# Kernel optimization log

Measured on AMD Instinct MI355X. Metric: run time of the kernel, lower is better.

## Reference

```python
import jax, jax.numpy as jnp
import numpy as np

E, T, K, H, I = 16, 512, 8, 2048, 1024  # experts, tokens, top-k, hidden, ffn half-width


def setup_inputs() -> dict:
    key = jax.random.key(0)
    ks = jax.random.split(key, 8)
    x = jax.random.normal(ks[0], (T, H), dtype=jnp.float32)
    expert_ids = jax.random.randint(ks[1], (T, K), 0, E, dtype=jnp.int32)
    # int8-valued weights stored as int32 (exactly representable)
    gmm1_weight = jax.random.randint(ks[2], (E, H, 2 * I), -127, 128, dtype=jnp.int32)
    gmm2_weight = jax.random.randint(ks[3], (E, I, H), -127, 128, dtype=jnp.int32)
    gmm1_weight_scale = jax.random.uniform(ks[4], (E, 2 * I), dtype=jnp.float32) * 1e-3
    gmm2_weight_scale = jax.random.uniform(ks[5], (E, H), dtype=jnp.float32) * 1e-3
    smooth_scales = jax.random.uniform(ks[6], (E, H), dtype=jnp.float32)
    expert_scales = jax.random.uniform(ks[7], (T, K), dtype=jnp.float32)
    return {"x": x, "expert_ids": expert_ids, "gmm1_weight": gmm1_weight,
            "gmm1_weight_scale": gmm1_weight_scale, "gmm2_weight": gmm2_weight,
            "gmm2_weight_scale": gmm2_weight_scale, "smooth_scales": smooth_scales,
            "expert_scales": expert_scales}


def _dynamic_quant(v):
    # per-token symmetric dynamic quant to int8 range (quant_mode=2 / quant_mode=1)
    s = jnp.max(jnp.abs(v), axis=-1, keepdims=True) / 127.0
    q = jnp.clip(jnp.round(v / s), -128.0, 127.0)  # kept in f32; values are exact small ints
    return q, s


def _grouped_mm(a, w, e_flat):
    # grouped GEMM: out[i] = a[i] @ w[e_flat[i]]. Disjoint expert masks -> masked full GEMMs summed.
    out = jnp.zeros((a.shape[0], w.shape[-1]), dtype=a.dtype)
    for e in range(w.shape[0]):
        mask = (e_flat == e)[:, None]
        out = out + jnp.where(mask, a, 0.0) @ w[e]
    return out


def reference(x, expert_ids, gmm1_weight, gmm1_weight_scale, gmm2_weight,
              gmm2_weight_scale, smooth_scales, expert_scales):
    # --- dispatch: per-token dynamic int8 quant + replicate each token K times ---
    xq, s0 = _dynamic_quant(x)                 # [T,H], [T,1]
    e_flat = expert_ids.reshape(-1)            # [T*K]
    xq_e = jnp.repeat(xq, K, axis=0)           # [T*K,H]
    s0_e = jnp.repeat(s0, K, axis=0)           # [T*K,1] == dynamic_scales / activation_scale
    w1 = gmm1_weight.astype(jnp.float32)       # int8 GEMM emulated exactly in f32
    w2 = gmm2_weight.astype(jnp.float32)
    # --- grouped GEMM 1 -> int32 accumulator values ---
    y1_i32 = _grouped_mm(xq_e, w1, e_flat)     # [T*K,2I]
    # --- fused dequant + SwiGLU (activate_left) + per-token dynamic requant ---
    y1f = y1_i32 * gmm1_weight_scale[e_flat] * s0_e
    act = jax.nn.silu(y1f[:, :I]) * y1f[:, I:]
    aq, s1 = _dynamic_quant(act)               # [T*K,I], [T*K,1]
    # --- grouped GEMM 2 + dequant (per-channel weight scale * per-token scale) ---
    y2_i32 = _grouped_mm(aq, w2, e_flat)       # [T*K,H]
    y2 = y2_i32 * gmm2_weight_scale[e_flat] * s1
    # --- combine: weighted sum over the K expert copies of each token ---
    out = jnp.einsum('tkh,tk->th', y2.reshape(T, K, H), expert_scales)
    return out
```

## Files before the change

kernel.cpp:

```cpp
#include <hip/hip_runtime.h>
#include <hip/hip_bf16.h>
#include <stdint.h>

#define E_   16
#define T_   512
#define KTOP 8
#define H_   2048
#define I_   1024
#define TK_  4096

typedef __attribute__((ext_vector_type(4))) int i32x4;

#define OFF_CNT     0
#define OFF_ROWMAX  4096
#define OFF_XQ      32768
#define OFF_S0      (OFF_XQ + T_*H_)
#define OFF_S1      (OFF_S0 + 4096)
#define OFF_LIST    (OFF_S1 + TK_*4)
#define OFF_ACT     (OFF_LIST + E_*TK_*4)
#define OFF_AQ      (OFF_ACT + (size_t)TK_*I_*4)
#define OFF_Y2      (OFF_AQ + (size_t)TK_*I_)

#define SCHEDB() __builtin_amdgcn_sched_barrier(0)
#define VMCNT26() asm volatile("s_waitcnt vmcnt(26)" ::: "memory")
#define LGKM0()   asm volatile("s_waitcnt lgkmcnt(0)" ::: "memory")
#define BAR()     __builtin_amdgcn_s_barrier()

__global__ void k_zero(unsigned int* __restrict__ p) {
  int i = blockIdx.x * 256 + threadIdx.x;
  if (i < 5120) p[i] = 0;
}

__global__ void k_quant(const float* __restrict__ x, signed char* __restrict__ xq,
                        float* __restrict__ s0, const int* __restrict__ eids,
                        unsigned int* __restrict__ counts, int* __restrict__ row_list) {
  int t = blockIdx.x, tid = threadIdx.x;
  if (tid < KTOP) {
    int e = eids[t * KTOP + tid];
    int pos = (int)atomicAdd(&counts[e], 1u);
    row_list[e * TK_ + pos] = t * KTOP + tid;
  }
  const float4* xr = (const float4*)(x + (size_t)t * H_);
  float4 a = xr[tid * 2 + 0], b = xr[tid * 2 + 1];
  float m = fmaxf(
      fmaxf(fmaxf(fabsf(a.x), fabsf(a.y)), fmaxf(fabsf(a.z), fabsf(a.w))),
      fmaxf(fmaxf(fabsf(b.x), fabsf(b.y)), fmaxf(fabsf(b.z), fabsf(b.w))));
  for (int o = 32; o > 0; o >>= 1) m = fmaxf(m, __shfl_xor(m, o));
  __shared__ float wm[4];
  if ((tid & 63) == 0) wm[tid >> 6] = m;
  __syncthreads();
  m = fmaxf(fmaxf(wm[0], wm[1]), fmaxf(wm[2], wm[3]));
  float s = m / 127.0f;
  if (!(s > 0.f)) s = 1.0f;
  if (tid == 0) s0[t] = s;
  float v[8] = {a.x, a.y, a.z, a.w, b.x, b.y, b.z, b.w};
  unsigned int lo = 0, hi = 0;
#pragma unroll
  for (int j = 0; j < 4; ++j) {
    float qf = fminf(fmaxf(rintf(v[j] / s), -128.f), 127.f);
    lo |= ((unsigned)((int)qf & 0xFF)) << (8 * j);
  }
#pragma unroll
  for (int j = 0; j < 4; ++j) {
    float qf = fminf(fmaxf(rintf(v[4 + j] / s), -128.f), 127.f);
    hi |= ((unsigned)((int)qf & 0xFF)) << (8 * j);
  }
  ((uint2*)(xq + (size_t)t * H_))[tid] = make_uint2(lo, hi);
}

#define BM_   320
#define WSTR  2048

#define PACKW(SRC, DST) do {                                              \
    i32x4 pk_;                                                            \
    _Pragma("unroll")                                                     \
    for (int d_ = 0; d_ < 4; ++d_)                                        \
      pk_[d_] = ((SRC)[4*d_] & 0xFF) | (((SRC)[4*d_+1] & 0xFF) << 8) |    \
                (((SRC)[4*d_+2] & 0xFF) << 16) | ((SRC)[4*d_+3] << 24);   \
    *(i32x4*)(DST) = pk_;                                                 \
  } while (0)

#define LOADB(BANK, TT)                                                   \
    _Pragma("unroll")                                                     \
    for (int j_ = 0; j_ < 16; ++j_)                                       \
      BANK[j_] = bsrc[(size_t)((TT) * 64 + j_) * WSTR];

#define LOADAR(BANK, TT)                                                  \
    _Pragma("unroll")                                                     \
    for (int i_ = 0; i_ < 5; ++i_)                                        \
      BANK[i_] = *(const i32x4*)(gA[i_] + (TT) * 64);

#define MFMAS(ABANK, P)                                                   \
    _Pragma("unroll")                                                     \
    for (int n_ = 0; n_ < 4; ++n_) {                                      \
      i32x4 bf_ = *(const i32x4*)(bsm + (P) * 4096 + l4 * 1024 +          \
                                  (n_ * 16 + l15) * 16);                  \
      _Pragma("unroll")                                                   \
      for (int i_ = 0; i_ < 5; ++i_)                                      \
        acc[i_][n_] = __builtin_amdgcn_mfma_i32_16x16x64_i8(              \
            ABANK[i_], bf_, acc[i_][n_], 0, 0, 0);                        \
    }

#define TILE(TT, P, ABANK, BBANK, PKBANK, NT, LAST) do {                  \
    int tn_ = (TT) + 2; if (tn_ > (NT) - 1) tn_ = (NT) - 1;               \
    SCHEDB();                                                             \
    LOADB(BBANK, tn_);                                                    \
    SCHEDB();                                                             \
    MFMAS(ABANK, P);                                                      \
    SCHEDB();                                                             \
    LOADAR(ABANK, tn_);                                                   \
    SCHEDB();                                                             \
    if (!(LAST)) {                                                        \
      VMCNT26(); SCHEDB();                                                \
      PACKW(PKBANK, bsm + ((P) ^ 1) * 4096 + bkg * 1024 + bc * 16);       \
      LGKM0(); BAR(); SCHEDB();                                           \
    }                                                                     \
  } while (0)

__launch_bounds__(256, 2)
__global__ void k_gemm1(const signed char* __restrict__ xq, const int* __restrict__ w1,
                        const float* __restrict__ ws1, const float* __restrict__ s0,
                        const unsigned int* __restrict__ counts,
                        const int* __restrict__ row_list,
                        float* __restrict__ act, unsigned int* __restrict__ rowmax) {
  __shared__ alignas(16) char bsm[2 * 4096];
  int e = blockIdx.y;
  int cnt = (int)counts[e];
  if (cnt == 0) return;
  int p0 = blockIdx.x * 32;
  const int* rl = row_list + e * TK_;
  const int* we = w1 + (size_t)e * H_ * (2 * I_);
  const float* wsc = ws1 + (size_t)e * (2 * I_);

  int tid = threadIdx.x, w = tid >> 6, lane = tid & 63;
  int l15 = lane & 15, l4 = lane >> 4;
  int bc = tid & 63, bkg = tid >> 6;
  int bgcol = (bc < 32) ? (p0 + bc) : (I_ + p0 + (bc - 32));
  const int* bsrc = we + (size_t)(bkg * 16) * WSTR + bgcol;

  const int NT = H_ / 64;
  int nch = (cnt + BM_ - 1) / BM_;
  for (int ch = 0; ch < nch; ++ch) {
    if (ch) { BAR(); }
    int rbase = ch * BM_;
    const signed char* gA[5];
#pragma unroll
    for (int i = 0; i < 5; ++i) {
      int gr = rbase + w * 80 + i * 16 + l15;
      int tok = rl[gr < cnt ? gr : 0] >> 3;
      gA[i] = xq + (size_t)tok * H_ + l4 * 16;
    }
    i32x4 acc[5][4];
#pragma unroll
    for (int i = 0; i < 5; ++i)
#pragma unroll
      for (int n = 0; n < 4; ++n) acc[i][n] = (i32x4)(0);

    i32x4 aR0[5], aR1[5];
    int bR0[16], bR1[16];
    SCHEDB();
    LOADB(bR0, 0);
    SCHEDB();
    LOADAR(aR0, 0);
    LOADAR(aR1, 1);
    SCHEDB();
    LOADB(bR1, 1);
    SCHEDB();
    VMCNT26(); SCHEDB();
    PACKW(bR0, bsm + bkg * 1024 + bc * 16);
    LGKM0(); BAR(); SCHEDB();

    for (int t = 0; t < NT; t += 2) {
      TILE(t,     0, aR0, bR0, bR1, NT, false);
      TILE(t + 1, 1, aR1, bR1, bR0, NT, (t + 2 >= NT));
    }

#pragma unroll
    for (int mi = 0; mi < 5; ++mi) {
#pragma unroll
      for (int r = 0; r < 4; ++r) {
        int gr = rbase + w * 80 + mi * 16 + l4 * 4 + r;
        bool valid = gr < cnt;
        int irow = rl[valid ? gr : 0];
        float s0v = s0[irow >> 3];
        float rowm = 0.f, av0 = 0.f, av1 = 0.f;
#pragma unroll
        for (int n = 0; n < 2; ++n) {
          int colL = p0 + n * 16 + l15;
          float yl = (float)acc[mi][n][r] * wsc[colL] * s0v;
          float yr = (float)acc[mi][n + 2][r] * wsc[I_ + colL] * s0v;
          float actv = (yl / (1.f + expf(-yl))) * yr;
          if (n == 0) av0 = actv; else av1 = actv;
          rowm = fmaxf(rowm, fabsf(actv));
        }
        rowm = fmaxf(rowm, __shfl_xor(rowm, 1));
        rowm = fmaxf(rowm, __shfl_xor(rowm, 2));
        rowm = fmaxf(rowm, __shfl_xor(rowm, 4));
        rowm = fmaxf(rowm, __shfl_xor(rowm, 8));
        if (valid) {
          act[(size_t)irow * I_ + p0 + l15] = av0;
          act[(size_t)irow * I_ + p0 + 16 + l15] = av1;
          if (l15 == 0) atomicMax(rowmax + irow, __float_as_uint(rowm));
        }
      }
    }
  }
}

__global__ void k_requant(const float* __restrict__ act, const unsigned int* __restrict__ rowmax,
                          signed char* __restrict__ aq, float* __restrict__ s1) {
  int i = blockIdx.x, tid = threadIdx.x;
  float m = __uint_as_float(rowmax[i]);
  float s = (m > 0.f) ? (m / 127.0f) : 1.0f;
  if (tid == 0) s1[i] = s;
  float4 v = ((const float4*)(act + (size_t)i * I_))[tid];
  float vv[4] = {v.x, v.y, v.z, v.w};
  unsigned int pk = 0;
#pragma unroll
  for (int j = 0; j < 4; ++j) {
    float qf = fminf(fmaxf(rintf(vv[j] / s), -128.f), 127.f);
    pk |= ((unsigned)((int)qf & 0xFF)) << (8 * j);
  }
  ((unsigned int*)(aq + (size_t)i * I_))[tid] = pk;
}

__launch_bounds__(256, 2)
__global__ void k_gemm2(const signed char* __restrict__ aq, const int* __restrict__ w2,
                        const float* __restrict__ ws2, const float* __restrict__ s1,
                        const float* __restrict__ es,
                        const unsigned int* __restrict__ counts,
                        const int* __restrict__ row_list,
                        __hip_bfloat16* __restrict__ y2h) {
  __shared__ alignas(16) char bsm[2 * 4096];
  int e = blockIdx.y;
  int cnt = (int)counts[e];
  if (cnt == 0) return;
  int n0 = blockIdx.x * 64;
  const int* rl = row_list + e * TK_;
  const int* we = w2 + (size_t)e * I_ * H_;
  const float* wsc = ws2 + (size_t)e * H_;

  int tid = threadIdx.x, w = tid >> 6, lane = tid & 63;
  int l15 = lane & 15, l4 = lane >> 4;
  int bc = tid & 63, bkg = tid >> 6;
  const int* bsrc = we + (size_t)(bkg * 16) * WSTR + n0 + bc;

  const int NT = I_ / 64;
  int nch = (cnt + BM_ - 1) / BM_;
  for (int ch = 0; ch < nch; ++ch) {
    if (ch) { BAR(); }
    int rbase = ch * BM_;
    const signed char* gA[5];
#pragma unroll
    for (int i = 0; i < 5; ++i) {
      int gr = rbase + w * 80 + i * 16 + l15;
      gA[i] = aq + (size_t)rl[gr < cnt ? gr : 0] * I_ + l4 * 16;
    }
    i32x4 acc[5][4];
#pragma unroll
    for (int i = 0; i < 5; ++i)
#pragma unroll
      for (int n = 0; n < 4; ++n) acc[i][n] = (i32x4)(0);

    i32x4 aR0[5], aR1[5];
    int bR0[16], bR1[16];
    SCHEDB();
    LOADB(bR0, 0);
    SCHEDB();
    LOADAR(aR0, 0);
    LOADAR(aR1, 1);
    SCHEDB();
    LOADB(bR1, 1);
    SCHEDB();
    VMCNT26(); SCHEDB();
    PACKW(bR0, bsm + bkg * 1024 + bc * 16);
    LGKM0(); BAR(); SCHEDB();

    for (int t = 0; t < NT; t += 2) {
      TILE(t,     0, aR0, bR0, bR1, NT, false);
      TILE(t + 1, 1, aR1, bR1, bR0, NT, (t + 2 >= NT));
    }

#pragma unroll
    for (int mi = 0; mi < 5; ++mi) {
#pragma unroll
      for (int r = 0; r < 4; ++r) {
        int gr = rbase + w * 80 + mi * 16 + l4 * 4 + r;
        if (gr < cnt) {
          int irow = rl[gr];
          float sc = s1[irow] * es[irow];
#pragma unroll
          for (int n = 0; n < 4; ++n) {
            int c = n0 + n * 16 + l15;
            float v = (float)acc[mi][n][r] * wsc[c] * sc;
            y2h[(size_t)irow * H_ + c] = __float2bfloat16(v);
          }
        }
      }
    }
  }
}

__global__ void k_combine(const __hip_bfloat16* __restrict__ y2h, float* __restrict__ out) {
  int idx = blockIdx.x * 256 + threadIdx.x;
  int t = idx >> 8;
  int h0 = (idx & 255) * 8;
  float s[8];
#pragma unroll
  for (int j = 0; j < 8; ++j) s[j] = 0.f;
#pragma unroll
  for (int k = 0; k < KTOP; ++k) {
    const __hip_bfloat16* p = y2h + ((size_t)(t * KTOP + k) * H_ + h0);
    uint4 u = *(const uint4*)p;
    const __hip_bfloat16* b = (const __hip_bfloat16*)&u;
#pragma unroll
    for (int j = 0; j < 8; ++j) s[j] += __bfloat162float(b[j]);
  }
  float4 o0 = make_float4(s[0], s[1], s[2], s[3]);
  float4 o1 = make_float4(s[4], s[5], s[6], s[7]);
  float4* dst = (float4*)(out + (size_t)t * H_ + h0);
  dst[0] = o0; dst[1] = o1;
}

extern "C" void kernel_launch(void* const* d_in, const int* in_sizes, int n_in,
                              void* d_out, int out_size, void* d_ws, size_t ws_size,
                              hipStream_t stream) {
  const float* x   = (const float*)d_in[0];
  const int*   eid = (const int*)d_in[1];
  const int*   w1  = (const int*)d_in[2];
  const float* ws1 = (const float*)d_in[3];
  const int*   w2  = (const int*)d_in[4];
  const float* ws2 = (const float*)d_in[5];
  const float* es  = (const float*)d_in[7];
  float* out = (float*)d_out;
  char* ws = (char*)d_ws;

  unsigned int*  counts   = (unsigned int*)(ws + OFF_CNT);
  unsigned int*  rowmax   = (unsigned int*)(ws + OFF_ROWMAX);
  signed char*   xq       = (signed char*)(ws + OFF_XQ);
  float*         s0       = (float*)(ws + OFF_S0);
  float*         s1       = (float*)(ws + OFF_S1);
  int*           row_list = (int*)(ws + OFF_LIST);
  float*         act      = (float*)(ws + OFF_ACT);
  signed char*   aq       = (signed char*)(ws + OFF_AQ);
  __hip_bfloat16* y2h     = (__hip_bfloat16*)(ws + OFF_Y2);

  k_zero<<<20, 256, 0, stream>>>((unsigned int*)ws);
  k_quant<<<T_, 256, 0, stream>>>(x, xq, s0, eid, counts, row_list);
  k_gemm1<<<dim3(32, E_), 256, 0, stream>>>(xq, w1, ws1, s0, counts, row_list, act, rowmax);
  k_requant<<<TK_, 256, 0, stream>>>(act, rowmax, aq, s1);
  k_gemm2<<<dim3(32, E_), 256, 0, stream>>>(aq, w2, ws2, s1, es, counts, row_list, y2h);
  k_combine<<<(T_ * H_ / 8) / 256, 256, 0, stream>>>(y2h, out);
}
```

Baseline: 183.4 us.

## Stage gathered A rows into LDS via direct global-to-LDS loads with 512-thread blocks

Both grouped GEMMs now use 512-thread blocks (8 waves, BM 384, 48 rows per wave). The gathered activation rows are copied straight into a double-buffered, XOR-swizzled LDS tile with global_load_lds, where previously each wave held them in registers. The B-weight load is split so each wave loads 8 rows and packs 8 bytes. The aim is lower register pressure, higher occupancy and more latency hiding for the A gather, at the cost of more LDS (56KB per block) and a more complex swizzle and wait scheme that could break correctness or limit residency. The chunk-start barrier was removed, which risks a race between chunks.

After: 290.5 us. 58.4% more time.

```diff
diff --git a/kernel.cpp b/kernel.cpp
--- a/kernel.cpp
+++ b/kernel.cpp
@@ -22,9 +22,15 @@
 #define OFF_Y2      (OFF_AQ + (size_t)TK_*I_)
 
 #define SCHEDB() __builtin_amdgcn_sched_barrier(0)
-#define VMCNT26() asm volatile("s_waitcnt vmcnt(26)" ::: "memory")
-#define LGKM0()   asm volatile("s_waitcnt lgkmcnt(0)" ::: "memory")
-#define BAR()     __builtin_amdgcn_s_barrier()
+#define VMCNT8() asm volatile("s_waitcnt vmcnt(8)" ::: "memory")
+#define LGKM0()  asm volatile("s_waitcnt lgkmcnt(0)" ::: "memory")
+#define BAR()    __builtin_amdgcn_s_barrier()
+
+__device__ __forceinline__ void g2l16(const void* g, void* l) {
+  __builtin_amdgcn_global_load_lds(
+      (const __attribute__((address_space(1))) void*)g,
+      (__attribute__((address_space(3))) void*)l, 16, 0, 0);
+}
 
 __global__ void k_zero(unsigned int* __restrict__ p) {
   int i = blockIdx.x * 256 + threadIdx.x;
@@ -68,62 +74,84 @@
   ((uint2*)(xq + (size_t)t * H_))[tid] = make_uint2(lo, hi);
 }
 
-#define BM_   320
-#define WSTR  2048
-
-#define PACKW(SRC, DST) do {                                              \
-    i32x4 pk_;                                                            \
+#define BM_    384
+#define WSTR   2048
+#define ABUFB  24576
+#define BBASE  49152
+#define LDSSZ  57344
+
+#define PACK8(SRC, DSTPTR) do {                                           \
+    uint2 u_;                                                             \
+    u_.x = ((SRC)[0] & 0xFF) | (((SRC)[1] & 0xFF) << 8) |                 \
+           (((SRC)[2] & 0xFF) << 16) | ((SRC)[3] << 24);                  \
+    u_.y = ((SRC)[4] & 0xFF) | (((SRC)[5] & 0xFF) << 8) |                 \
+           (((SRC)[6] & 0xFF) << 16) | ((SRC)[7] << 24);                  \
+    *(uint2*)(DSTPTR) = u_;                                               \
+  } while (0)
+
+#define LOADB8(BANK, TT)                                                  \
     _Pragma("unroll")                                                     \
-    for (int d_ = 0; d_ < 4; ++d_)                                        \
-      pk_[d_] = ((SRC)[4*d_] & 0xFF) | (((SRC)[4*d_+1] & 0xFF) << 8) |    \
-                (((SRC)[4*d_+2] & 0xFF) << 16) | ((SRC)[4*d_+3] << 24);   \
-    *(i32x4*)(DST) = pk_;                                                 \
-  } while (0)
-
-#define LOADB(BANK, TT)                                                   \
+    for (int j_ = 0; j_ < 8; ++j_)                                        \
+      BANK[j_] = bsrc[(size_t)((TT) * 64 + j_) * WSTR];
+
+#define STAGEA(TT, BUF)                                                   \
     _Pragma("unroll")                                                     \
-    for (int j_ = 0; j_ < 16; ++j_)                                       \
-      BANK[j_] = bsrc[(size_t)((TT) * 64 + j_) * WSTR];
-
-#define LOADAR(BANK, TT)                                                  \
-    _Pragma("unroll")                                                     \
-    for (int i_ = 0; i_ < 5; ++i_)                                        \
-      BANK[i_] = *(const i32x4*)(gA[i_] + (TT) * 64);
-
-#define MFMAS(ABANK, P)                                                   \
-    _Pragma("unroll")                                                     \
-    for (int n_ = 0; n_ < 4; ++n_) {                                      \
-      i32x4 bf_ = *(const i32x4*)(bsm + (P) * 4096 + l4 * 1024 +          \
-                                  (n_ * 16 + l15) * 16);                  \
+    for (int s_ = 0; s_ < 3; ++s_)                                        \
+      g2l16(gAr[s_] + (TT) * 64, smem + (BUF) * ABUFB + s_ * 8192 + w * 1024);
+
+#define MFMAS(P)                                                          \
+    do {                                                                  \
+      i32x4 af_[3];                                                       \
       _Pragma("unroll")                                                   \
-      for (int i_ = 0; i_ < 5; ++i_)                                      \
-        acc[i_][n_] = __builtin_amdgcn_mfma_i32_16x16x64_i8(              \
-            ABANK[i_], bf_, acc[i_][n_], 0, 0, 0);                        \
-    }
-
-#define TILE(TT, P, ABANK, BBANK, PKBANK, NT, LAST) do {                  \
-    int tn_ = (TT) + 2; if (tn_ > (NT) - 1) tn_ = (NT) - 1;               \
-    SCHEDB();                                                             \
-    LOADB(BBANK, tn_);                                                    \
-    SCHEDB();                                                             \
-    MFMAS(ABANK, P);                                                      \
-    SCHEDB();                                                             \
-    LOADAR(ABANK, tn_);                                                   \
+      for (int mi_ = 0; mi_ < 3; ++mi_)                                   \
+        af_[mi_] = *(const i32x4*)(smem + (P) * ABUFB + aoff[mi_]);       \
+      _Pragma("unroll")                                                   \
+      for (int n_ = 0; n_ < 4; ++n_) {                                    \
+        i32x4 bf_ = *(const i32x4*)(smem + BBASE + (P) * 4096 +           \
+                                    l4 * 1024 + (n_ * 16 + l15) * 16);    \
+        _Pragma("unroll")                                                 \
+        for (int mi_ = 0; mi_ < 3; ++mi_)                                 \
+          acc[mi_][n_] = __builtin_amdgcn_mfma_i32_16x16x64_i8(           \
+              af_[mi_], bf_, acc[mi_][n_], 0, 0, 0);                      \
+      }                                                                   \
+    } while (0)
+
+#define TILE(TT, P, BBANK, PKBANK, NT, LAST) do {                         \
+    if (!(LAST)) { STAGEA((TT) + 1, (P) ^ 1); }                           \
     SCHEDB();                                                             \
     if (!(LAST)) {                                                        \
-      VMCNT26(); SCHEDB();                                                \
-      PACKW(PKBANK, bsm + ((P) ^ 1) * 4096 + bkg * 1024 + bc * 16);       \
+      int tn_ = (TT) + 2; if (tn_ > (NT) - 1) tn_ = (NT) - 1;             \
+      LOADB8(BBANK, tn_);                                                 \
+    }                                                                     \
+    SCHEDB();                                                             \
+    MFMAS(P);                                                             \
+    SCHEDB();                                                             \
+    if (!(LAST)) {                                                        \
+      VMCNT8(); SCHEDB();                                                 \
+      PACK8(PKBANK, smem + BBASE + ((P) ^ 1) * 4096 + pdst);              \
       LGKM0(); BAR(); SCHEDB();                                           \
     }                                                                     \
   } while (0)
 
-__launch_bounds__(256, 2)
+#define GEMM_PRO()                                                        \
+    SCHEDB();                                                             \
+    STAGEA(0, 0);                                                         \
+    SCHEDB();                                                             \
+    LOADB8(bRA, 0);                                                       \
+    SCHEDB();                                                             \
+    LOADB8(bRB, 1);                                                       \
+    SCHEDB();                                                             \
+    VMCNT8(); SCHEDB();                                                   \
+    PACK8(bRA, smem + BBASE + pdst);                                      \
+    LGKM0(); BAR(); SCHEDB();
+
+__launch_bounds__(512, 4)
 __global__ void k_gemm1(const signed char* __restrict__ xq, const int* __restrict__ w1,
                         const float* __restrict__ ws1, const float* __restrict__ s0,
                         const unsigned int* __restrict__ counts,
                         const int* __restrict__ row_list,
                         float* __restrict__ act, unsigned int* __restrict__ rowmax) {
-  __shared__ alignas(16) char bsm[2 * 4096];
+  __shared__ alignas(16) char smem[LDSSZ];
   int e = blockIdx.y;
   int cnt = (int)counts[e];
   if (cnt == 0) return;
@@ -134,52 +162,52 @@
 
   int tid = threadIdx.x, w = tid >> 6, lane = tid & 63;
   int l15 = lane & 15, l4 = lane >> 4;
-  int bc = tid & 63, bkg = tid >> 6;
-  int bgcol = (bc < 32) ? (p0 + bc) : (I_ + p0 + (bc - 32));
-  const int* bsrc = we + (size_t)(bkg * 16) * WSTR + bgcol;
+
+  int bgcol = (lane < 32) ? (p0 + lane) : (I_ + p0 + (lane - 32));
+  const int* bsrc = we + (size_t)(w * 8) * WSTR + bgcol;
+  const int pdst = (w >> 1) * 1024 + lane * 16 + (w & 1) * 8;
+
+  int aR[3], akc;
+  akc = ((tid >> 2) & 3) ^ ((tid >> 4) & 3);
+#pragma unroll
+  for (int s = 0; s < 3; ++s) aR[s] = s * 128 + ((tid >> 4) << 2) + (tid & 3);
+
+  int aoff[3];
+#pragma unroll
+  for (int mi = 0; mi < 3; ++mi) {
+    int R = w * 48 + mi * 16 + l15;
+    aoff[mi] = ((R >> 2) << 8) + ((l4 ^ ((R >> 2) & 3)) << 6) + ((R & 3) << 4);
+  }
 
   const int NT = H_ / 64;
   int nch = (cnt + BM_ - 1) / BM_;
   for (int ch = 0; ch < nch; ++ch) {
-    if (ch) { BAR(); }
     int rbase = ch * BM_;
-    const signed char* gA[5];
-#pragma unroll
-    for (int i = 0; i < 5; ++i) {
-      int gr = rbase + w * 80 + i * 16 + l15;
+    const signed char* gAr[3];
+#pragma unroll
+    for (int s = 0; s < 3; ++s) {
+      int gr = rbase + aR[s];
       int tok = rl[gr < cnt ? gr : 0] >> 3;
-      gA[i] = xq + (size_t)tok * H_ + l4 * 16;
-    }
-    i32x4 acc[5][4];
-#pragma unroll
-    for (int i = 0; i < 5; ++i)
+      gAr[s] = xq + (size_t)tok * H_ + akc * 16;
+    }
+    i32x4 acc[3][4];
+#pragma unroll
+    for (int i = 0; i < 3; ++i)
 #pragma unroll
       for (int n = 0; n < 4; ++n) acc[i][n] = (i32x4)(0);
 
-    i32x4 aR0[5], aR1[5];
-    int bR0[16], bR1[16];
-    SCHEDB();
-    LOADB(bR0, 0);
-    SCHEDB();
-    LOADAR(aR0, 0);
-    LOADAR(aR1, 1);
-    SCHEDB();
-    LOADB(bR1, 1);
-    SCHEDB();
-    VMCNT26(); SCHEDB();
-    PACKW(bR0, bsm + bkg * 1024 + bc * 16);
-    LGKM0(); BAR(); SCHEDB();
-
+    int bRA[8], bRB[8];
+    GEMM_PRO();
     for (int t = 0; t < NT; t += 2) {
-      TILE(t,     0, aR0, bR0, bR1, NT, false);
-      TILE(t + 1, 1, aR1, bR1, bR0, NT, (t + 2 >= NT));
-    }
-
-#pragma unroll
-    for (int mi = 0; mi < 5; ++mi) {
+      TILE(t,     0, bRA, bRB, NT, false);
+      TILE(t + 1, 1, bRB, bRA, NT, (t + 2 >= NT));
+    }
+
+#pragma unroll
+    for (int mi = 0; mi < 3; ++mi) {
 #pragma unroll
       for (int r = 0; r < 4; ++r) {
-        int gr = rbase + w * 80 + mi * 16 + l4 * 4 + r;
+        int gr = rbase + w * 48 + mi * 16 + l4 * 4 + r;
         bool valid = gr < cnt;
         int irow = rl[valid ? gr : 0];
         float s0v = s0[irow >> 3];
@@ -224,14 +252,14 @@
   ((unsigned int*)(aq + (size_t)i * I_))[tid] = pk;
 }
 
-__launch_bounds__(256, 2)
+__launch_bounds__(512, 4)
 __global__ void k_gemm2(const signed char* __restrict__ aq, const int* __restrict__ w2,
                         const float* __restrict__ ws2, const float* __restrict__ s1,
                         const float* __restrict__ es,
                         const unsigned int* __restrict__ counts,
                         const int* __restrict__ row_list,
                         __hip_bfloat16* __restrict__ y2h) {
-  __shared__ alignas(16) char bsm[2 * 4096];
+  __shared__ alignas(16) char smem[LDSSZ];
   int e = blockIdx.y;
   int cnt = (int)counts[e];
   if (cnt == 0) return;
@@ -242,50 +270,50 @@
 
   int tid = threadIdx.x, w = tid >> 6, lane = tid & 63;
   int l15 = lane & 15, l4 = lane >> 4;
-  int bc = tid & 63, bkg = tid >> 6;
-  const int* bsrc = we + (size_t)(bkg * 16) * WSTR + n0 + bc;
+
+  const int* bsrc = we + (size_t)(w * 8) * WSTR + n0 + lane;
+  const int pdst = (w >> 1) * 1024 + lane * 16 + (w & 1) * 8;
+
+  int aR[3], akc;
+  akc = ((tid >> 2) & 3) ^ ((tid >> 4) & 3);
+#pragma unroll
+  for (int s = 0; s < 3; ++s) aR[s] = s * 128 + ((tid >> 4) << 2) + (tid & 3);
+
+  int aoff[3];
+#pragma unroll
+  for (int mi = 0; mi < 3; ++mi) {
+    int R = w * 48 + mi * 16 + l15;
+    aoff[mi] = ((R >> 2) << 8) + ((l4 ^ ((R >> 2) & 3)) << 6) + ((R & 3) << 4);
+  }
 
   const int NT = I_ / 64;
   int nch = (cnt + BM_ - 1) / BM_;
   for (int ch = 0; ch < nch; ++ch) {
-    if (ch) { BAR(); }
     int rbase = ch * BM_;
-    const signed char* gA[5];
-#pragma unroll
-    for (int i = 0; i < 5; ++i) {
-      int gr = rbase + w * 80 + i * 16 + l15;
-      gA[i] = aq + (size_t)rl[gr < cnt ? gr : 0] * I_ + l4 * 16;
-    }
-    i32x4 acc[5][4];
-#pragma unroll
-    for (int i = 0; i < 5; ++i)
+    const signed char* gAr[3];
+#pragma unroll
+    for (int s = 0; s < 3; ++s) {
+      int gr = rbase + aR[s];
+      gAr[s] = aq + (size_t)rl[gr < cnt ? gr : 0] * I_ + akc * 16;
+    }
+    i32x4 acc[3][4];
+#pragma unroll
+    for (int i = 0; i < 3; ++i)
 #pragma unroll
       for (int n = 0; n < 4; ++n) acc[i][n] = (i32x4)(0);
 
-    i32x4 aR0[5], aR1[5];
-    int bR0[16], bR1[16];
-    SCHEDB();
-    LOADB(bR0, 0);
-    SCHEDB();
-    LOADAR(aR0, 0);
-    LOADAR(aR1, 1);
-    SCHEDB();
-    LOADB(bR1, 1);
-    SCHEDB();
-    VMCNT26(); SCHEDB();
-    PACKW(bR0, bsm + bkg * 1024 + bc * 16);
-    LGKM0(); BAR(); SCHEDB();
-
+    int bRA[8], bRB[8];
+    GEMM_PRO();
     for (int t = 0; t < NT; t += 2) {
-      TILE(t,     0, aR0, bR0, bR1, NT, false);
-      TILE(t + 1, 1, aR1, bR1, bR0, NT, (t + 2 >= NT));
-    }
-
-#pragma unroll
-    for (int mi = 0; mi < 5; ++mi) {
+      TILE(t,     0, bRA, bRB, NT, false);
+      TILE(t + 1, 1, bRB, bRA, NT, (t + 2 >= NT));
+    }
+
+#pragma unroll
+    for (int mi = 0; mi < 3; ++mi) {
 #pragma unroll
       for (int r = 0; r < 4; ++r) {
-        int gr = rbase + w * 80 + mi * 16 + l4 * 4 + r;
+        int gr = rbase + w * 48 + mi * 16 + l4 * 4 + r;
         if (gr < cnt) {
           int irow = rl[gr];
           float sc = s1[irow] * es[irow];
@@ -347,8 +375,8 @@
 
   k_zero<<<20, 256, 0, stream>>>((unsigned int*)ws);
   k_quant<<<T_, 256, 0, stream>>>(x, xq, s0, eid, counts, row_list);
-  k_gemm1<<<dim3(32, E_), 256, 0, stream>>>(xq, w1, ws1, s0, counts, row_list, act, rowmax);
+  k_gemm1<<<dim3(32, E_), 512, 0, stream>>>(xq, w1, ws1, s0, counts, row_list, act, rowmax);
   k_requant<<<TK_, 256, 0, stream>>>(act, rowmax, aq, s1);
-  k_gemm2<<<dim3(32, E_), 256, 0, stream>>>(aq, w2, ws2, s1, es, counts, row_list, y2h);
+  k_gemm2<<<dim3(32, E_), 512, 0, stream>>>(aq, w2, ws2, s1, es, counts, row_list, y2h);
   k_combine<<<(T_ * H_ / 8) / 256, 256, 0, stream>>>(y2h, out);
 }
```

## Halve GEMM N-tile width to double grid and raise occupancy

Applied to the files above, without the earlier changes.

Both grouped GEMM kernels now compute 32-wide (gemm1: 16 left + 16 right columns) output tiles instead of 64, doubling the grid to 64x16 blocks and raising launch bounds to 4 waves per SIMD. Each thread loads 8 weight rows instead of 16, with a new LDS packing layout and a matching vmcnt wait. The final tile also skips its redundant prefetch loads. The aim is to fill more CUs and hide memory latency, at the cost of reloading the A (activation) rows twice as often per expert.

Result: slower. 361.9 us (+97.3%).

```diff
diff --git a/kernel.cpp b/kernel.cpp
--- a/kernel.cpp
+++ b/kernel.cpp
@@ -21,8 +21,8 @@
 #define OFF_AQ      (OFF_ACT + (size_t)TK_*I_*4)
 #define OFF_Y2      (OFF_AQ + (size_t)TK_*I_)
 
-#define SCHEDB() __builtin_amdgcn_sched_barrier(0)
-#define VMCNT26() asm volatile("s_waitcnt vmcnt(26)" ::: "memory")
+#define SCHEDB()  __builtin_amdgcn_sched_barrier(0)
+#define VMCNT18() asm volatile("s_waitcnt vmcnt(18)" ::: "memory")
 #define LGKM0()   asm volatile("s_waitcnt lgkmcnt(0)" ::: "memory")
 #define BAR()     __builtin_amdgcn_s_barrier()
 
@@ -71,18 +71,18 @@
 #define BM_   320
 #define WSTR  2048
 
-#define PACKW(SRC, DST) do {                                              \
-    i32x4 pk_;                                                            \
+#define PACK8(SRC, DSTPTR) do {                                           \
+    uint2 u_;                                                             \
+    u_.x = ((SRC)[0] & 0xFF) | (((SRC)[1] & 0xFF) << 8) |                 \
+           (((SRC)[2] & 0xFF) << 16) | ((SRC)[3] << 24);                  \
+    u_.y = ((SRC)[4] & 0xFF) | (((SRC)[5] & 0xFF) << 8) |                 \
+           (((SRC)[6] & 0xFF) << 16) | ((SRC)[7] << 24);                  \
+    *(uint2*)(DSTPTR) = u_;                                               \
+  } while (0)
+
+#define LOADB8(BANK, TT)                                                  \
     _Pragma("unroll")                                                     \
-    for (int d_ = 0; d_ < 4; ++d_)                                        \
-      pk_[d_] = ((SRC)[4*d_] & 0xFF) | (((SRC)[4*d_+1] & 0xFF) << 8) |    \
-                (((SRC)[4*d_+2] & 0xFF) << 16) | ((SRC)[4*d_+3] << 24);   \
-    *(i32x4*)(DST) = pk_;                                                 \
-  } while (0)
-
-#define LOADB(BANK, TT)                                                   \
-    _Pragma("unroll")                                                     \
-    for (int j_ = 0; j_ < 16; ++j_)                                       \
+    for (int j_ = 0; j_ < 8; ++j_)                                        \
       BANK[j_] = bsrc[(size_t)((TT) * 64 + j_) * WSTR];
 
 #define LOADAR(BANK, TT)                                                  \
@@ -92,8 +92,8 @@
 
 #define MFMAS(ABANK, P)                                                   \
     _Pragma("unroll")                                                     \
-    for (int n_ = 0; n_ < 4; ++n_) {                                      \
-      i32x4 bf_ = *(const i32x4*)(bsm + (P) * 4096 + l4 * 1024 +          \
+    for (int n_ = 0; n_ < 2; ++n_) {                                      \
+      i32x4 bf_ = *(const i32x4*)(bsm + (P) * 2048 + l4 * 512 +           \
                                   (n_ * 16 + l15) * 16);                  \
       _Pragma("unroll")                                                   \
       for (int i_ = 0; i_ < 5; ++i_)                                      \
@@ -101,42 +101,57 @@
             ABANK[i_], bf_, acc[i_][n_], 0, 0, 0);                        \
     }
 
-#define TILE(TT, P, ABANK, BBANK, PKBANK, NT, LAST) do {                  \
+#define TILE(TT, P, BBANK, PKBANK, ABANK, NT, LAST) do {                  \
     int tn_ = (TT) + 2; if (tn_ > (NT) - 1) tn_ = (NT) - 1;               \
-    SCHEDB();                                                             \
-    LOADB(BBANK, tn_);                                                    \
+    if (!(LAST)) { LOADB8(BBANK, tn_); }                                  \
     SCHEDB();                                                             \
     MFMAS(ABANK, P);                                                      \
     SCHEDB();                                                             \
-    LOADAR(ABANK, tn_);                                                   \
+    if (!(LAST)) { LOADAR(ABANK, tn_); }                                  \
     SCHEDB();                                                             \
     if (!(LAST)) {                                                        \
-      VMCNT26(); SCHEDB();                                                \
-      PACKW(PKBANK, bsm + ((P) ^ 1) * 4096 + bkg * 1024 + bc * 16);       \
+      VMCNT18(); SCHEDB();                                                \
+      PACK8(PKBANK, bsm + ((P) ^ 1) * 2048 + pdst);                       \
       LGKM0(); BAR(); SCHEDB();                                           \
     }                                                                     \
   } while (0)
 
-__launch_bounds__(256, 2)
+#define GEMM_PRO()                                                        \
+    SCHEDB();                                                             \
+    LOADB8(bRA, 0);                                                       \
+    SCHEDB();                                                             \
+    LOADAR(aR0, 0);                                                       \
+    SCHEDB();                                                             \
+    LOADB8(bRB, 1);                                                       \
+    SCHEDB();                                                             \
+    LOADAR(aR1, 1);                                                       \
+    SCHEDB();                                                             \
+    VMCNT18(); SCHEDB();                                                  \
+    PACK8(bRA, bsm + pdst);                                               \
+    LGKM0(); BAR(); SCHEDB();
+
+__launch_bounds__(256, 4)
 __global__ void k_gemm1(const signed char* __restrict__ xq, const int* __restrict__ w1,
                         const float* __restrict__ ws1, const float* __restrict__ s0,
                         const unsigned int* __restrict__ counts,
                         const int* __restrict__ row_list,
                         float* __restrict__ act, unsigned int* __restrict__ rowmax) {
-  __shared__ alignas(16) char bsm[2 * 4096];
+  __shared__ alignas(16) char bsm[2 * 2048];
   int e = blockIdx.y;
   int cnt = (int)counts[e];
   if (cnt == 0) return;
-  int p0 = blockIdx.x * 32;
+  int p0 = blockIdx.x * 16;
   const int* rl = row_list + e * TK_;
   const int* we = w1 + (size_t)e * H_ * (2 * I_);
   const float* wsc = ws1 + (size_t)e * (2 * I_);
 
   int tid = threadIdx.x, w = tid >> 6, lane = tid & 63;
   int l15 = lane & 15, l4 = lane >> 4;
-  int bc = tid & 63, bkg = tid >> 6;
-  int bgcol = (bc < 32) ? (p0 + bc) : (I_ + p0 + (bc - 32));
-  const int* bsrc = we + (size_t)(bkg * 16) * WSTR + bgcol;
+
+  int bc = tid & 31, kg = tid >> 5;
+  int bgcol = (bc < 16) ? (p0 + bc) : (I_ + p0 + (bc - 16));
+  const int* bsrc = we + (size_t)(kg * 8) * WSTR + bgcol;
+  const int pdst = (kg >> 1) * 512 + bc * 16 + (kg & 1) * 8;
 
   const int NT = H_ / 64;
   int nch = (cnt + BM_ - 1) / BM_;
@@ -150,29 +165,16 @@
       int tok = rl[gr < cnt ? gr : 0] >> 3;
       gA[i] = xq + (size_t)tok * H_ + l4 * 16;
     }
-    i32x4 acc[5][4];
-#pragma unroll
-    for (int i = 0; i < 5; ++i)
-#pragma unroll
-      for (int n = 0; n < 4; ++n) acc[i][n] = (i32x4)(0);
+    i32x4 acc[5][2];
+#pragma unroll
+    for (int i = 0; i < 5; ++i) { acc[i][0] = (i32x4)(0); acc[i][1] = (i32x4)(0); }
 
     i32x4 aR0[5], aR1[5];
-    int bR0[16], bR1[16];
-    SCHEDB();
-    LOADB(bR0, 0);
-    SCHEDB();
-    LOADAR(aR0, 0);
-    LOADAR(aR1, 1);
-    SCHEDB();
-    LOADB(bR1, 1);
-    SCHEDB();
-    VMCNT26(); SCHEDB();
-    PACKW(bR0, bsm + bkg * 1024 + bc * 16);
-    LGKM0(); BAR(); SCHEDB();
-
+    int bRA[8], bRB[8];
+    GEMM_PRO();
     for (int t = 0; t < NT; t += 2) {
-      TILE(t,     0, aR0, bR0, bR1, NT, false);
-      TILE(t + 1, 1, aR1, bR1, bR0, NT, (t + 2 >= NT));
+      TILE(t,     0, bRA, bRB, aR0, NT, false);
+      TILE(t + 1, 1, bRB, bRA, aR1, NT, (t + 2 >= NT));
     }
 
 #pragma unroll
@@ -183,23 +185,16 @@
         bool valid = gr < cnt;
         int irow = rl[valid ? gr : 0];
         float s0v = s0[irow >> 3];
-        float rowm = 0.f, av0 = 0.f, av1 = 0.f;
-#pragma unroll
-        for (int n = 0; n < 2; ++n) {
-          int colL = p0 + n * 16 + l15;
-          float yl = (float)acc[mi][n][r] * wsc[colL] * s0v;
-          float yr = (float)acc[mi][n + 2][r] * wsc[I_ + colL] * s0v;
-          float actv = (yl / (1.f + expf(-yl))) * yr;
-          if (n == 0) av0 = actv; else av1 = actv;
-          rowm = fmaxf(rowm, fabsf(actv));
-        }
+        float yl = (float)acc[mi][0][r] * wsc[p0 + l15] * s0v;
+        float yr = (float)acc[mi][1][r] * wsc[I_ + p0 + l15] * s0v;
+        float actv = (yl / (1.f + expf(-yl))) * yr;
+        float rowm = fabsf(actv);
         rowm = fmaxf(rowm, __shfl_xor(rowm, 1));
         rowm = fmaxf(rowm, __shfl_xor(rowm, 2));
         rowm = fmaxf(rowm, __shfl_xor(rowm, 4));
         rowm = fmaxf(rowm, __shfl_xor(rowm, 8));
         if (valid) {
-          act[(size_t)irow * I_ + p0 + l15] = av0;
-          act[(size_t)irow * I_ + p0 + 16 + l15] = av1;
+          act[(size_t)irow * I_ + p0 + l15] = actv;
           if (l15 == 0) atomicMax(rowmax + irow, __float_as_uint(rowm));
         }
       }
@@ -224,26 +219,28 @@
   ((unsigned int*)(aq + (size_t)i * I_))[tid] = pk;
 }
 
-__launch_bounds__(256, 2)
+__launch_bounds__(256, 4)
 __global__ void k_gemm2(const signed char* __restrict__ aq, const int* __restrict__ w2,
                         const float* __restrict__ ws2, const float* __restrict__ s1,
                         const float* __restrict__ es,
                         const unsigned int* __restrict__ counts,
                         const int* __restrict__ row_list,
                         __hip_bfloat16* __restrict__ y2h) {
-  __shared__ alignas(16) char bsm[2 * 4096];
+  __shared__ alignas(16) char bsm[2 * 2048];
   int e = blockIdx.y;
   int cnt = (int)counts[e];
   if (cnt == 0) return;
-  int n0 = blockIdx.x * 64;
+  int n0 = blockIdx.x * 32;
   const int* rl = row_list + e * TK_;
   const int* we = w2 + (size_t)e * I_ * H_;
   const float* wsc = ws2 + (size_t)e * H_;
 
   int tid = threadIdx.x, w = tid >> 6, lane = tid & 63;
   int l15 = lane & 15, l4 = lane >> 4;
-  int bc = tid & 63, bkg = tid >> 6;
-  const int* bsrc = we + (size_t)(bkg * 16) * WSTR + n0 + bc;
+
+  int bc = tid & 31, kg = tid >> 5;
+  const int* bsrc = we + (size_t)(kg * 8) * WSTR + n0 + bc;
+  const int pdst = (kg >> 1) * 512 + bc * 16 + (kg & 1) * 8;
 
   const int NT = I_ / 64;
   int nch = (cnt + BM_ - 1) / BM_;
@@ -256,29 +253,16 @@
       int gr = rbase + w * 80 + i * 16 + l15;
       gA[i] = aq + (size_t)rl[gr < cnt ? gr : 0] * I_ + l4 * 16;
     }
-    i32x4 acc[5][4];
-#pragma unroll
-    for (int i = 0; i < 5; ++i)
-#pragma unroll
-      for (int n = 0; n < 4; ++n) acc[i][n] = (i32x4)(0);
+    i32x4 acc[5][2];
+#pragma unroll
+    for (int i = 0; i < 5; ++i) { acc[i][0] = (i32x4)(0); acc[i][1] = (i32x4)(0); }
 
     i32x4 aR0[5], aR1[5];
-    int bR0[16], bR1[16];
-    SCHEDB();
-    LOADB(bR0, 0);
-    SCHEDB();
-    LOADAR(aR0, 0);
-    LOADAR(aR1, 1);
-    SCHEDB();
-    LOADB(bR1, 1);
-    SCHEDB();
-    VMCNT26(); SCHEDB();
-    PACKW(bR0, bsm + bkg * 1024 + bc * 16);
-    LGKM0(); BAR(); SCHEDB();
-
+    int bRA[8], bRB[8];
+    GEMM_PRO();
     for (int t = 0; t < NT; t += 2) {
-      TILE(t,     0, aR0, bR0, bR1, NT, false);
-      TILE(t + 1, 1, aR1, bR1, bR0, NT, (t + 2 >= NT));
+      TILE(t,     0, bRA, bRB, aR0, NT, false);
+      TILE(t + 1, 1, bRB, bRA, aR1, NT, (t + 2 >= NT));
     }
 
 #pragma unroll
@@ -290,7 +274,7 @@
           int irow = rl[gr];
           float sc = s1[irow] * es[irow];
 #pragma unroll
-          for (int n = 0; n < 4; ++n) {
+          for (int n = 0; n < 2; ++n) {
             int c = n0 + n * 16 + l15;
             float v = (float)acc[mi][n][r] * wsc[c] * sc;
             y2h[(size_t)irow * H_ + c] = __float2bfloat16(v);
@@ -347,8 +331,8 @@
 
   k_zero<<<20, 256, 0, stream>>>((unsigned int*)ws);
   k_quant<<<T_, 256, 0, stream>>>(x, xq, s0, eid, counts, row_list);
-  k_gemm1<<<dim3(32, E_), 256, 0, stream>>>(xq, w1, ws1, s0, counts, row_list, act, rowmax);
+  k_gemm1<<<dim3(64, E_), 256, 0, stream>>>(xq, w1, ws1, s0, counts, row_list, act, rowmax);
   k_requant<<<TK_, 256, 0, stream>>>(act, rowmax, aq, s1);
-  k_gemm2<<<dim3(32, E_), 256, 0, stream>>>(aq, w2, ws2, s1, es, counts, row_list, y2h);
+  k_gemm2<<<dim3(64, E_), 256, 0, stream>>>(aq, w2, ws2, s1, es, counts, row_list, y2h);
   k_combine<<<(T_ * H_ / 8) / 256, 256, 0, stream>>>(y2h, out);
 }
```

## Restructure grouped GEMMs to 512-thread blocks with single-buffer LDS and syncthreads pipeline

Applied to the files above, without the earlier changes.

Both grouped GEMM kernels move from 256-thread blocks with 320-row chunks to 512-thread blocks with 256-row chunks. Each wave now owns 32 rows, which shrinks the per-thread accumulator and register banks and raises the launch-bounds occupancy target. The hand-tuned double-buffered LDS pipeline with explicit vmcnt waits is replaced by a single padded (80-byte stride) B tile, register double-buffering and __syncthreads barriers. This gives more waves to hide latency and should reduce LDS bank conflicts, at the cost of more barriers per K-tile and less A-operand reuse per wave.

New measurement: 202.2 us. 1.1x slower.

```diff
diff --git a/kernel.cpp b/kernel.cpp
--- a/kernel.cpp
+++ b/kernel.cpp
@@ -22,9 +22,6 @@
 #define OFF_Y2      (OFF_AQ + (size_t)TK_*I_)
 
 #define SCHEDB() __builtin_amdgcn_sched_barrier(0)
-#define VMCNT26() asm volatile("s_waitcnt vmcnt(26)" ::: "memory")
-#define LGKM0()   asm volatile("s_waitcnt lgkmcnt(0)" ::: "memory")
-#define BAR()     __builtin_amdgcn_s_barrier()
 
 __global__ void k_zero(unsigned int* __restrict__ p) {
   int i = blockIdx.x * 256 + threadIdx.x;
@@ -68,62 +65,57 @@
   ((uint2*)(xq + (size_t)t * H_))[tid] = make_uint2(lo, hi);
 }
 
-#define BM_   320
+#define BM_   256
 #define WSTR  2048
 
-#define PACKW(SRC, DST) do {                                              \
-    i32x4 pk_;                                                            \
-    _Pragma("unroll")                                                     \
-    for (int d_ = 0; d_ < 4; ++d_)                                        \
-      pk_[d_] = ((SRC)[4*d_] & 0xFF) | (((SRC)[4*d_+1] & 0xFF) << 8) |    \
-                (((SRC)[4*d_+2] & 0xFF) << 16) | ((SRC)[4*d_+3] << 24);   \
-    *(i32x4*)(DST) = pk_;                                                 \
-  } while (0)
+#define PACKU2(SRC) (make_uint2(                                          \
+    ((SRC)[0] & 0xFF) | (((SRC)[1] & 0xFF) << 8) |                        \
+    (((SRC)[2] & 0xFF) << 16) | ((SRC)[3] << 24),                         \
+    ((SRC)[4] & 0xFF) | (((SRC)[5] & 0xFF) << 8) |                        \
+    (((SRC)[6] & 0xFF) << 16) | ((SRC)[7] << 24)))
 
 #define LOADB(BANK, TT)                                                   \
     _Pragma("unroll")                                                     \
-    for (int j_ = 0; j_ < 16; ++j_)                                       \
-      BANK[j_] = bsrc[(size_t)((TT) * 64 + j_) * WSTR];
-
-#define LOADAR(BANK, TT)                                                  \
+    for (int j_ = 0; j_ < 8; ++j_)                                        \
+      BANK[j_] = bsrc[(size_t)((TT) * 64 + brow0 + j_) * WSTR];
+
+#define LOADA(BANK, TT)                                                   \
     _Pragma("unroll")                                                     \
-    for (int i_ = 0; i_ < 5; ++i_)                                        \
-      BANK[i_] = *(const i32x4*)(gA[i_] + (TT) * 64);
-
-#define MFMAS(ABANK, P)                                                   \
+    for (int mi_ = 0; mi_ < 2; ++mi_)                                     \
+      BANK[mi_] = *(const i32x4*)(gA[mi_] + (TT) * 64);
+
+#define WRITEB(BANK) do { *(uint2*)bdst = PACKU2(BANK); } while (0)
+
+#define MFMAS(ABANK)                                                      \
     _Pragma("unroll")                                                     \
-    for (int n_ = 0; n_ < 4; ++n_) {                                      \
-      i32x4 bf_ = *(const i32x4*)(bsm + (P) * 4096 + l4 * 1024 +          \
-                                  (n_ * 16 + l15) * 16);                  \
+    for (int f_ = 0; f_ < 4; ++f_) {                                      \
+      i32x4 bf_ = *(const i32x4*)(bsm + (f_ * 16 + l15) * 80 + l4 * 16);  \
       _Pragma("unroll")                                                   \
-      for (int i_ = 0; i_ < 5; ++i_)                                      \
-        acc[i_][n_] = __builtin_amdgcn_mfma_i32_16x16x64_i8(              \
-            ABANK[i_], bf_, acc[i_][n_], 0, 0, 0);                        \
-    }
-
-#define TILE(TT, P, ABANK, BBANK, PKBANK, NT, LAST) do {                  \
-    int tn_ = (TT) + 2; if (tn_ > (NT) - 1) tn_ = (NT) - 1;               \
+      for (int mi_ = 0; mi_ < 2; ++mi_)                                   \
+        acc[mi_][f_] = __builtin_amdgcn_mfma_i32_16x16x64_i8(             \
+            ABANK[mi_], bf_, acc[mi_][f_], 0, 0, 0);                      \
+    }
+
+#define TILE2(TT)                                                         \
+    __syncthreads();                                                      \
+    WRITEB(b0);                                                           \
+    LOADB(b1, (TT) + 1); LOADA(a1, (TT) + 1); SCHEDB();                   \
+    __syncthreads();                                                      \
+    MFMAS(a0);                                                            \
+    __syncthreads();                                                      \
+    WRITEB(b1);                                                           \
+    if ((TT) + 2 < NT) { LOADB(b0, (TT) + 2); LOADA(a0, (TT) + 2); }      \
     SCHEDB();                                                             \
-    LOADB(BBANK, tn_);                                                    \
-    SCHEDB();                                                             \
-    MFMAS(ABANK, P);                                                      \
-    SCHEDB();                                                             \
-    LOADAR(ABANK, tn_);                                                   \
-    SCHEDB();                                                             \
-    if (!(LAST)) {                                                        \
-      VMCNT26(); SCHEDB();                                                \
-      PACKW(PKBANK, bsm + ((P) ^ 1) * 4096 + bkg * 1024 + bc * 16);       \
-      LGKM0(); BAR(); SCHEDB();                                           \
-    }                                                                     \
-  } while (0)
-
-__launch_bounds__(256, 2)
+    __syncthreads();                                                      \
+    MFMAS(a1);
+
+__launch_bounds__(512, 4)
 __global__ void k_gemm1(const signed char* __restrict__ xq, const int* __restrict__ w1,
                         const float* __restrict__ ws1, const float* __restrict__ s0,
                         const unsigned int* __restrict__ counts,
                         const int* __restrict__ row_list,
                         float* __restrict__ act, unsigned int* __restrict__ rowmax) {
-  __shared__ alignas(16) char bsm[2 * 4096];
+  __shared__ alignas(16) char bsm[64 * 80];
   int e = blockIdx.y;
   int cnt = (int)counts[e];
   if (cnt == 0) return;
@@ -134,52 +126,38 @@
 
   int tid = threadIdx.x, w = tid >> 6, lane = tid & 63;
   int l15 = lane & 15, l4 = lane >> 4;
-  int bc = tid & 63, bkg = tid >> 6;
-  int bgcol = (bc < 32) ? (p0 + bc) : (I_ + p0 + (bc - 32));
-  const int* bsrc = we + (size_t)(bkg * 16) * WSTR + bgcol;
+
+  int bcol = (lane < 32) ? (p0 + lane) : (I_ + p0 + (lane - 32));
+  const int* bsrc = we + bcol;
+  const int brow0 = w * 8;
+  char* bdst = bsm + lane * 80 + w * 8;
 
   const int NT = H_ / 64;
-  int nch = (cnt + BM_ - 1) / BM_;
-  for (int ch = 0; ch < nch; ++ch) {
-    if (ch) { BAR(); }
+  for (int ch = 0; ch * BM_ < cnt; ++ch) {
     int rbase = ch * BM_;
-    const signed char* gA[5];
-#pragma unroll
-    for (int i = 0; i < 5; ++i) {
-      int gr = rbase + w * 80 + i * 16 + l15;
+    const signed char* gA[2];
+#pragma unroll
+    for (int mi = 0; mi < 2; ++mi) {
+      int gr = rbase + w * 32 + mi * 16 + l15;
       int tok = rl[gr < cnt ? gr : 0] >> 3;
-      gA[i] = xq + (size_t)tok * H_ + l4 * 16;
-    }
-    i32x4 acc[5][4];
-#pragma unroll
-    for (int i = 0; i < 5; ++i)
+      gA[mi] = xq + (size_t)tok * H_ + l4 * 16;
+    }
+    i32x4 acc[2][4];
+#pragma unroll
+    for (int i = 0; i < 2; ++i)
 #pragma unroll
       for (int n = 0; n < 4; ++n) acc[i][n] = (i32x4)(0);
 
-    i32x4 aR0[5], aR1[5];
-    int bR0[16], bR1[16];
-    SCHEDB();
-    LOADB(bR0, 0);
-    SCHEDB();
-    LOADAR(aR0, 0);
-    LOADAR(aR1, 1);
-    SCHEDB();
-    LOADB(bR1, 1);
-    SCHEDB();
-    VMCNT26(); SCHEDB();
-    PACKW(bR0, bsm + bkg * 1024 + bc * 16);
-    LGKM0(); BAR(); SCHEDB();
-
-    for (int t = 0; t < NT; t += 2) {
-      TILE(t,     0, aR0, bR0, bR1, NT, false);
-      TILE(t + 1, 1, aR1, bR1, bR0, NT, (t + 2 >= NT));
-    }
-
-#pragma unroll
-    for (int mi = 0; mi < 5; ++mi) {
+    int b0[8], b1[8];
+    i32x4 a0[2], a1[2];
+    LOADB(b0, 0); LOADA(a0, 0); SCHEDB();
+    for (int t = 0; t < NT; t += 2) { TILE2(t); }
+
+#pragma unroll
+    for (int mi = 0; mi < 2; ++mi) {
 #pragma unroll
       for (int r = 0; r < 4; ++r) {
-        int gr = rbase + w * 80 + mi * 16 + l4 * 4 + r;
+        int gr = rbase + w * 32 + mi * 16 + l4 * 4 + r;
         bool valid = gr < cnt;
         int irow = rl[valid ? gr : 0];
         float s0v = s0[irow >> 3];
@@ -224,14 +202,14 @@
   ((unsigned int*)(aq + (size_t)i * I_))[tid] = pk;
 }
 
-__launch_bounds__(256, 2)
+__launch_bounds__(512, 4)
 __global__ void k_gemm2(const signed char* __restrict__ aq, const int* __restrict__ w2,
                         const float* __restrict__ ws2, const float* __restrict__ s1,
                         const float* __restrict__ es,
                         const unsigned int* __restrict__ counts,
                         const int* __restrict__ row_list,
                         __hip_bfloat16* __restrict__ y2h) {
-  __shared__ alignas(16) char bsm[2 * 4096];
+  __shared__ alignas(16) char bsm[64 * 80];
   int e = blockIdx.y;
   int cnt = (int)counts[e];
   if (cnt == 0) return;
@@ -242,50 +220,36 @@
 
   int tid = threadIdx.x, w = tid >> 6, lane = tid & 63;
   int l15 = lane & 15, l4 = lane >> 4;
-  int bc = tid & 63, bkg = tid >> 6;
-  const int* bsrc = we + (size_t)(bkg * 16) * WSTR + n0 + bc;
+
+  const int* bsrc = we + n0 + lane;
+  const int brow0 = w * 8;
+  char* bdst = bsm + lane * 80 + w * 8;
 
   const int NT = I_ / 64;
-  int nch = (cnt + BM_ - 1) / BM_;
-  for (int ch = 0; ch < nch; ++ch) {
-    if (ch) { BAR(); }
+  for (int ch = 0; ch * BM_ < cnt; ++ch) {
     int rbase = ch * BM_;
-    const signed char* gA[5];
-#pragma unroll
-    for (int i = 0; i < 5; ++i) {
-      int gr = rbase + w * 80 + i * 16 + l15;
-      gA[i] = aq + (size_t)rl[gr < cnt ? gr : 0] * I_ + l4 * 16;
-    }
-    i32x4 acc[5][4];
-#pragma unroll
-    for (int i = 0; i < 5; ++i)
+    const signed char* gA[2];
+#pragma unroll
+    for (int mi = 0; mi < 2; ++mi) {
+      int gr = rbase + w * 32 + mi * 16 + l15;
+      gA[mi] = aq + (size_t)rl[gr < cnt ? gr : 0] * I_ + l4 * 16;
+    }
+    i32x4 acc[2][4];
+#pragma unroll
+    for (int i = 0; i < 2; ++i)
 #pragma unroll
       for (int n = 0; n < 4; ++n) acc[i][n] = (i32x4)(0);
 
-    i32x4 aR0[5], aR1[5];
-    int bR0[16], bR1[16];
-    SCHEDB();
-    LOADB(bR0, 0);
-    SCHEDB();
-    LOADAR(aR0, 0);
-    LOADAR(aR1, 1);
-    SCHEDB();
-    LOADB(bR1, 1);
-    SCHEDB();
-    VMCNT26(); SCHEDB();
-    PACKW(bR0, bsm + bkg * 1024 + bc * 16);
-    LGKM0(); BAR(); SCHEDB();
-
-    for (int t = 0; t < NT; t += 2) {
-      TILE(t,     0, aR0, bR0, bR1, NT, false);
-      TILE(t + 1, 1, aR1, bR1, bR0, NT, (t + 2 >= NT));
-    }
-
-#pragma unroll
-    for (int mi = 0; mi < 5; ++mi) {
+    int b0[8], b1[8];
+    i32x4 a0[2], a1[2];
+    LOADB(b0, 0); LOADA(a0, 0); SCHEDB();
+    for (int t = 0; t < NT; t += 2) { TILE2(t); }
+
+#pragma unroll
+    for (int mi = 0; mi < 2; ++mi) {
 #pragma unroll
       for (int r = 0; r < 4; ++r) {
-        int gr = rbase + w * 80 + mi * 16 + l4 * 4 + r;
+        int gr = rbase + w * 32 + mi * 16 + l4 * 4 + r;
         if (gr < cnt) {
           int irow = rl[gr];
           float sc = s1[irow] * es[irow];
@@ -347,8 +311,8 @@
 
   k_zero<<<20, 256, 0, stream>>>((unsigned int*)ws);
   k_quant<<<T_, 256, 0, stream>>>(x, xq, s0, eid, counts, row_list);
-  k_gemm1<<<dim3(32, E_), 256, 0, stream>>>(xq, w1, ws1, s0, counts, row_list, act, rowmax);
+  k_gemm1<<<dim3(32, E_), 512, 0, stream>>>(xq, w1, ws1, s0, counts, row_list, act, rowmax);
   k_requant<<<TK_, 256, 0, stream>>>(act, rowmax, aq, s1);
-  k_gemm2<<<dim3(32, E_), 256, 0, stream>>>(aq, w2, ws2, s1, es, counts, row_list, y2h);
+  k_gemm2<<<dim3(32, E_), 512, 0, stream>>>(aq, w2, ws2, s1, es, counts, row_list, y2h);
   k_combine<<<(T_ * H_ / 8) / 256, 256, 0, stream>>>(y2h, out);
 }
```
